# Kernel optimization log

Hardware: AMD Instinct MI355X
Metric: run time of the kernel (lower is better)

## Reference

```python
import jax, jax.numpy as jnp
import numpy as np

EPS = 0.001   # EPSILON2
T1 = 1.0
T2 = 100.0
DISC = 16     # number of discrete features
B, F, K1, K2 = 524288, 16, 16, 8


def _enforce(v):
    # Enforced autograd fn: forward = max(v, EPS), backward = identity (STE)
    return v + jax.lax.stop_gradient(jnp.maximum(v, EPS) - v)


def _soft_bin(cont, interval, i_min):
    """cont: [B,F]; interval: [F,K]; i_min: [F]. Vectorized over features/bins.
    Returns (STE one-hot out [B, F*K], kmeans_loss scalar)."""
    # bin centers = i_min + running cumsum of (enforced) gaps -> [F,K]
    centers = i_min[:, None] + jnp.cumsum(_enforce(interval), axis=1)
    d = (cont[:, :, None] - centers[None, :, :]) ** 2          # [B,F,K]
    s1 = jax.nn.softmax(-T1 * d, axis=-1)                      # kmeans softmax
    kmeans_loss = jnp.sum(jnp.mean(jnp.sum(d * s1, axis=-1), axis=0))
    s2 = jax.nn.softmax(-T2 * d, axis=-1)                      # sharp softmax
    oh = jax.nn.one_hot(jnp.argmax(s2, axis=-1), d.shape[-1], dtype=s2.dtype)
    out = s2 + jax.lax.stop_gradient(oh - s2)                  # STE one-hot
    return out.reshape(cont.shape[0], -1), kmeans_loss


def setup_inputs() -> dict:
    key = jax.random.key(0)
    k1, k2, k3 = jax.random.split(key, 3)
    x = jax.random.uniform(k1, (B, DISC + F), dtype=jnp.float32)
    interval = jax.random.uniform(k2, (F, K1), dtype=jnp.float32,
                                  minval=0.01, maxval=0.12)
    interval2 = jax.random.uniform(k3, (F, K2), dtype=jnp.float32,
                                   minval=0.02, maxval=0.2)
    i_min = jnp.zeros((F,), dtype=jnp.float32)
    return {"x": x, "interval": interval, "interval2": interval2, "i_min": i_min}


def reference(x, interval, interval2, i_min):
    x_disc, cont = x[:, :DISC], x[:, DISC:]
    out1, loss1 = _soft_bin(cont, interval, i_min)
    out2, loss2 = _soft_bin(cont, interval2, i_min)
    total_out = jnp.concatenate([x_disc, out1, out2], axis=1)  # [B, DISC+F*(K1+K2)]
    return total_out, loss1 + loss2
```

## Files before the change

### kernel.cpp

```cpp
#include <hip/hip_runtime.h>


typedef float vfloat4 __attribute__((ext_vector_type(4)));

constexpr int kB      = 524288;
constexpr int kF      = 16;
constexpr int kK1     = 16;
constexpr int kK2     = 8;
constexpr int kRowIn  = 32;
constexpr int kRowOut = 400;
constexpr float kEps  = 0.001f;
constexpr int kTPB    = 256;
constexpr int kGrid   = kB / kTPB;
constexpr int kXStride = 17;

template <int K>
__device__ __forceinline__ int soft_argmax_loss(const float* __restrict__ dd,
                                                double& lacc)
{
#pragma clang fp contract(off)
    float se = 0.f, sde = 0.f;
#pragma unroll
    for (int k = 0; k < K; ++k) {
        float e = __expf(-dd[k]);
        se += e; sde += dd[k] * e;
    }
    lacc += (double)(sde / se);

    float z[K];
#pragma unroll
    for (int k = 0; k < K; ++k) z[k] = -100.0f * dd[k];
    float m = z[0]; int kmax = 0;
#pragma unroll
    for (int k = 1; k < K; ++k) {
        if (z[k] > m) { m = z[k]; kmax = k; }
    }

    bool cand = false;
#pragma unroll
    for (int k = 0; k < K; ++k)
        cand |= (k < kmax) & (z[k] >= m - 2.4e-7f);
    if (cand) {
        float e2[K]; float ss = 0.f;
        for (int k = 0; k < K; ++k) { e2[k] = expf(z[k] - m); ss += e2[k]; }
        int km = 0; float pmax = e2[0] / ss;
        for (int k = 1; k < K; ++k) {
            float p = e2[k] / ss;
            if (p > pmax) { pmax = p; km = k; }
        }
        kmax = km;
    }
    return kmax;
}

__global__ __launch_bounds__(kTPB) void binlayer_main(
    const float* __restrict__ x,
    const float* __restrict__ interval,
    const float* __restrict__ interval2,
    const float* __restrict__ i_min,
    float* __restrict__ out,
    double* __restrict__ partial)
{
#pragma clang fp contract(off)
    __shared__ float sC1[kF][kK1];
    __shared__ float sC2[kF][kK2];
    __shared__ float sCont[kTPB * kXStride];
    __shared__ unsigned char sIdx[kTPB * kF];
    __shared__ double sL[kTPB / 64];

    const int tid = threadIdx.x;

    if (tid < kF) {
        const float base = i_min[tid];
        float run = 0.f;
        for (int k = 0; k < kK1; ++k) {
            run += fmaxf(interval[tid * kK1 + k], kEps);
            sC1[tid][k] = base + run;
        }
        run = 0.f;
        for (int k = 0; k < kK2; ++k) {
            run += fmaxf(interval2[tid * kK2 + k], kEps);
            sC2[tid][k] = base + run;
        }
    }

    const long long rowBase = (long long)blockIdx.x * kTPB;
    const vfloat4* __restrict__ xin4 = (const vfloat4*)(x + rowBase * kRowIn);
    vfloat4* __restrict__ o4 = (vfloat4*)(out + rowBase * kRowOut);

#pragma unroll
    for (int i = 0; i < 4; ++i) {
        int flat = i * kTPB + tid;
        int r = flat >> 2, c = flat & 3;
        vfloat4 v = xin4[r * 8 + 4 + c];
        float* p = &sCont[r * kXStride + c * 4];
        p[0] = v.x; p[1] = v.y; p[2] = v.z; p[3] = v.w;
    }

#pragma unroll
    for (int i = 0; i < 4; ++i) {
        int flat = i * kTPB + tid;
        int r = flat >> 2, c = flat & 3;
        vfloat4 v = xin4[r * 8 + c];
        __builtin_nontemporal_store(v, &o4[r * 100 + c]);
    }

    __syncthreads();

    double lacc = 0.0;
    const float* __restrict__ myc = &sCont[tid * kXStride];

#pragma unroll 1
    for (int f = 0; f < kF; ++f) {
        const float c = myc[f];

        float dd1[kK1];
#pragma unroll
        for (int k = 0; k < kK1; ++k) { float t = c - sC1[f][k]; dd1[k] = t * t; }
        int k1 = soft_argmax_loss<kK1>(dd1, lacc);

        float dd2[kK2];
#pragma unroll
        for (int k = 0; k < kK2; ++k) { float t = c - sC2[f][k]; dd2[k] = t * t; }
        int k2 = soft_argmax_loss<kK2>(dd2, lacc);

        sIdx[tid * kF + f] = (unsigned char)(k1 | (k2 << 4));
    }

#pragma unroll
    for (int off = 32; off > 0; off >>= 1) lacc += __shfl_down(lacc, off);
    if ((tid & 63) == 0) sL[tid >> 6] = lacc;

    __syncthreads();

    if (tid == 0) partial[blockIdx.x] = sL[0] + sL[1] + sL[2] + sL[3];

#pragma unroll 4
    for (int i = 0; i < 96; ++i) {
        unsigned idx = (unsigned)(i * kTPB + tid);
        unsigned r = idx / 96u;
        unsigned c = idx - r * 96u;
        vfloat4 o;
        if (c < 64u) {
            unsigned f = c >> 2, q = (c & 3u) * 4u;
            unsigned k = sIdx[r * kF + f] & 15u;
            o.x = (k == q + 0u) ? 1.f : 0.f;
            o.y = (k == q + 1u) ? 1.f : 0.f;
            o.z = (k == q + 2u) ? 1.f : 0.f;
            o.w = (k == q + 3u) ? 1.f : 0.f;
        } else {
            unsigned u = c - 64u, f = u >> 1, q = (u & 1u) * 4u;
            unsigned k = (unsigned)(sIdx[r * kF + f]) >> 4;
            o.x = (k == q + 0u) ? 1.f : 0.f;
            o.y = (k == q + 1u) ? 1.f : 0.f;
            o.z = (k == q + 2u) ? 1.f : 0.f;
            o.w = (k == q + 3u) ? 1.f : 0.f;
        }
        __builtin_nontemporal_store(o, &o4[r * 100u + 4u + c]);
    }
}

__global__ __launch_bounds__(256) void binlayer_finalize(
    const double* __restrict__ partial,
    float* __restrict__ out)
{
    __shared__ double sL[4];
    const int tid = threadIdx.x;
    double s = 0.0;
#pragma unroll
    for (int i = 0; i < kGrid / 256; ++i)
        s += partial[i * 256 + tid];
#pragma unroll
    for (int off = 32; off > 0; off >>= 1) s += __shfl_down(s, off);
    if ((tid & 63) == 0) sL[tid >> 6] = s;
    __syncthreads();
    if (tid == 0)
        out[(long long)kB * kRowOut] =
            (float)((sL[0] + sL[1] + sL[2] + sL[3]) * (1.0 / (double)kB));
}

extern "C" void kernel_launch(void* const* d_in, const int* in_sizes, int n_in,
                              void* d_out, int out_size, void* d_ws, size_t ws_size,
                              hipStream_t stream)
{
    const float* x    = (const float*)d_in[0];
    const float* itv1 = (const float*)d_in[1];
    const float* itv2 = (const float*)d_in[2];
    const float* imin = (const float*)d_in[3];
    float* out = (float*)d_out;
    double* partial = (double*)d_ws;

    binlayer_main<<<kGrid, kTPB, 0, stream>>>(x, itv1, itv2, imin, out, partial);
    binlayer_finalize<<<1, 256, 0, stream>>>(partial, out);
}
```

Measured before the change: 908.6 us.

## Split compute and one-hot expansion into separate kernels via packed index buffer

Splits the fused kernel into a compute kernel that writes 16 bytes of packed bin indices per row to workspace, and an expand kernel that writes the full contiguous output rows. Each phase can then run at its own occupancy, and the store phase no longer waits on the compute-heavy phase. Output stores become fully contiguous per block, since the x_disc copy is merged into the expansion loop, and they switch from nontemporal to normal stores. The cost is an extra launch, an extra read of x, and 8 MB of round-trip index traffic. A fused fallback is kept for when the workspace is too small.

```diff
diff --git a/kernel.cpp b/kernel.cpp
--- a/kernel.cpp
+++ b/kernel.cpp
@@ -13,6 +13,7 @@
 constexpr int kTPB    = 256;
 constexpr int kGrid   = kB / kTPB;
 constexpr int kXStride = 17;
+constexpr int kWStride = 5;
 
 template <int K>
 __device__ __forceinline__ int soft_argmax_loss(const float* __restrict__ dd,
@@ -35,7 +36,6 @@
     for (int k = 1; k < K; ++k) {
         if (z[k] > m) { m = z[k]; kmax = k; }
     }
-
     bool cand = false;
 #pragma unroll
     for (int k = 0; k < K; ++k)
@@ -53,7 +53,141 @@
     return kmax;
 }
 
-__global__ __launch_bounds__(kTPB) void binlayer_main(
+__device__ __forceinline__ void load_centers(
+    const float* __restrict__ interval, const float* __restrict__ interval2,
+    const float* __restrict__ i_min, int tid,
+    float (*sC1)[kK1], float (*sC2)[kK2])
+{
+#pragma clang fp contract(off)
+    if (tid < kF) {
+        const float base = i_min[tid];
+        float run = 0.f;
+        for (int k = 0; k < kK1; ++k) {
+            run += fmaxf(interval[tid * kK1 + k], kEps);
+            sC1[tid][k] = base + run;
+        }
+        run = 0.f;
+        for (int k = 0; k < kK2; ++k) {
+            run += fmaxf(interval2[tid * kK2 + k], kEps);
+            sC2[tid][k] = base + run;
+        }
+    }
+}
+
+__global__ __launch_bounds__(kTPB) void binlayer_compute(
+    const float* __restrict__ x,
+    const float* __restrict__ interval,
+    const float* __restrict__ interval2,
+    const float* __restrict__ i_min,
+    uint4* __restrict__ idxbuf,
+    double* __restrict__ partial)
+{
+#pragma clang fp contract(off)
+    __shared__ float sC1[kF][kK1];
+    __shared__ float sC2[kF][kK2];
+    __shared__ float sCont[kTPB * kXStride];
+    __shared__ double sL[kTPB / 64];
+
+    const int tid = threadIdx.x;
+    load_centers(interval, interval2, i_min, tid, sC1, sC2);
+
+    const long long rowBase = (long long)blockIdx.x * kTPB;
+    const vfloat4* __restrict__ xin4 = (const vfloat4*)(x + rowBase * kRowIn);
+
+#pragma unroll
+    for (int i = 0; i < 4; ++i) {
+        int flat = i * kTPB + tid;
+        int r = flat >> 2, c = flat & 3;
+        vfloat4 v = xin4[r * 8 + 4 + c];
+        float* p = &sCont[r * kXStride + c * 4];
+        p[0] = v.x; p[1] = v.y; p[2] = v.z; p[3] = v.w;
+    }
+    __syncthreads();
+
+    double lacc = 0.0;
+    const float* __restrict__ myc = &sCont[tid * kXStride];
+    unsigned w[4] = {0u, 0u, 0u, 0u};
+
+#pragma unroll 1
+    for (int f = 0; f < kF; ++f) {
+        const float c = myc[f];
+        float dd1[kK1];
+#pragma unroll
+        for (int k = 0; k < kK1; ++k) { float t = c - sC1[f][k]; dd1[k] = t * t; }
+        int k1 = soft_argmax_loss<kK1>(dd1, lacc);
+        float dd2[kK2];
+#pragma unroll
+        for (int k = 0; k < kK2; ++k) { float t = c - sC2[f][k]; dd2[k] = t * t; }
+        int k2 = soft_argmax_loss<kK2>(dd2, lacc);
+        w[f >> 2] |= (unsigned)(k1 | (k2 << 4)) << (8 * (f & 3));
+    }
+
+    idxbuf[rowBase + tid] = make_uint4(w[0], w[1], w[2], w[3]);
+
+#pragma unroll
+    for (int off = 32; off > 0; off >>= 1) lacc += __shfl_down(lacc, off);
+    if ((tid & 63) == 0) sL[tid >> 6] = lacc;
+    __syncthreads();
+    if (tid == 0) partial[blockIdx.x] = sL[0] + sL[1] + sL[2] + sL[3];
+}
+
+__global__ __launch_bounds__(kTPB) void binlayer_expand(
+    const float* __restrict__ x,
+    const uint4* __restrict__ idxbuf,
+    float* __restrict__ out)
+{
+    __shared__ float sX[kTPB * kXStride];
+    __shared__ unsigned sW[kTPB * kWStride];
+
+    const int tid = threadIdx.x;
+    const long long rowBase = (long long)blockIdx.x * kTPB;
+    const vfloat4* __restrict__ xin4 = (const vfloat4*)(x + rowBase * kRowIn);
+    vfloat4* __restrict__ o4 = (vfloat4*)(out + rowBase * kRowOut);
+
+    {
+        uint4 v = idxbuf[rowBase + tid];
+        unsigned* p = &sW[tid * kWStride];
+        p[0] = v.x; p[1] = v.y; p[2] = v.z; p[3] = v.w;
+    }
+#pragma unroll
+    for (int i = 0; i < 4; ++i) {
+        int flat = i * kTPB + tid;
+        int r = flat >> 2, c = flat & 3;
+        vfloat4 v = xin4[r * 8 + c];
+        float* p = &sX[r * kXStride + c * 4];
+        p[0] = v.x; p[1] = v.y; p[2] = v.z; p[3] = v.w;
+    }
+    __syncthreads();
+
+#pragma unroll 4
+    for (int i = 0; i < 100; ++i) {
+        unsigned idx = (unsigned)(i * kTPB + tid);
+        unsigned r = idx / 100u;
+        unsigned c = idx - r * 100u;
+        vfloat4 o;
+        if (c < 4u) {
+            const float* p = &sX[r * kXStride + c * 4u];
+            o.x = p[0]; o.y = p[1]; o.z = p[2]; o.w = p[3];
+        } else if (c < 68u) {
+            unsigned u = c - 4u, f = u >> 2, q = (u & 3u) * 4u;
+            unsigned k = (sW[r * kWStride + (f >> 2)] >> (8u * (f & 3u))) & 15u;
+            o.x = (k == q + 0u) ? 1.f : 0.f;
+            o.y = (k == q + 1u) ? 1.f : 0.f;
+            o.z = (k == q + 2u) ? 1.f : 0.f;
+            o.w = (k == q + 3u) ? 1.f : 0.f;
+        } else {
+            unsigned u = c - 68u, f = u >> 1, q = (u & 1u) * 4u;
+            unsigned k = (sW[r * kWStride + (f >> 2)] >> (8u * (f & 3u) + 4u)) & 15u;
+            o.x = (k == q + 0u) ? 1.f : 0.f;
+            o.y = (k == q + 1u) ? 1.f : 0.f;
+            o.z = (k == q + 2u) ? 1.f : 0.f;
+            o.w = (k == q + 3u) ? 1.f : 0.f;
+        }
+        o4[idx] = o;
+    }
+}
+
+__global__ __launch_bounds__(kTPB) void binlayer_fused(
     const float* __restrict__ x,
     const float* __restrict__ interval,
     const float* __restrict__ interval2,
@@ -64,99 +198,72 @@
 #pragma clang fp contract(off)
     __shared__ float sC1[kF][kK1];
     __shared__ float sC2[kF][kK2];
-    __shared__ float sCont[kTPB * kXStride];
+    __shared__ float sX[kTPB * 33];
     __shared__ unsigned char sIdx[kTPB * kF];
     __shared__ double sL[kTPB / 64];
 
     const int tid = threadIdx.x;
-
-    if (tid < kF) {
-        const float base = i_min[tid];
-        float run = 0.f;
-        for (int k = 0; k < kK1; ++k) {
-            run += fmaxf(interval[tid * kK1 + k], kEps);
-            sC1[tid][k] = base + run;
-        }
-        run = 0.f;
-        for (int k = 0; k < kK2; ++k) {
-            run += fmaxf(interval2[tid * kK2 + k], kEps);
-            sC2[tid][k] = base + run;
-        }
-    }
+    load_centers(interval, interval2, i_min, tid, sC1, sC2);
 
     const long long rowBase = (long long)blockIdx.x * kTPB;
     const vfloat4* __restrict__ xin4 = (const vfloat4*)(x + rowBase * kRowIn);
-    vfloat4* __restrict__ o4 = (vfloat4*)(out + rowBase * kRowOut);
-
-#pragma unroll
-    for (int i = 0; i < 4; ++i) {
+#pragma unroll
+    for (int i = 0; i < 8; ++i) {
         int flat = i * kTPB + tid;
-        int r = flat >> 2, c = flat & 3;
-        vfloat4 v = xin4[r * 8 + 4 + c];
-        float* p = &sCont[r * kXStride + c * 4];
+        vfloat4 v = xin4[flat];
+        int r = flat >> 3, c4 = flat & 7;
+        float* p = &sX[r * 33 + c4 * 4];
         p[0] = v.x; p[1] = v.y; p[2] = v.z; p[3] = v.w;
     }
-
-#pragma unroll
-    for (int i = 0; i < 4; ++i) {
-        int flat = i * kTPB + tid;
-        int r = flat >> 2, c = flat & 3;
-        vfloat4 v = xin4[r * 8 + c];
-        __builtin_nontemporal_store(v, &o4[r * 100 + c]);
-    }
-
     __syncthreads();
 
     double lacc = 0.0;
-    const float* __restrict__ myc = &sCont[tid * kXStride];
-
+    const float* __restrict__ myc = &sX[tid * 33 + 16];
 #pragma unroll 1
     for (int f = 0; f < kF; ++f) {
         const float c = myc[f];
-
         float dd1[kK1];
 #pragma unroll
         for (int k = 0; k < kK1; ++k) { float t = c - sC1[f][k]; dd1[k] = t * t; }
         int k1 = soft_argmax_loss<kK1>(dd1, lacc);
-
         float dd2[kK2];
 #pragma unroll
         for (int k = 0; k < kK2; ++k) { float t = c - sC2[f][k]; dd2[k] = t * t; }
         int k2 = soft_argmax_loss<kK2>(dd2, lacc);
-
         sIdx[tid * kF + f] = (unsigned char)(k1 | (k2 << 4));
     }
-
 #pragma unroll
     for (int off = 32; off > 0; off >>= 1) lacc += __shfl_down(lacc, off);
     if ((tid & 63) == 0) sL[tid >> 6] = lacc;
-
-    __syncthreads();
-
+    __syncthreads();
     if (tid == 0) partial[blockIdx.x] = sL[0] + sL[1] + sL[2] + sL[3];
 
-#pragma unroll 4
-    for (int i = 0; i < 96; ++i) {
+    vfloat4* __restrict__ o4 = (vfloat4*)(out + rowBase * kRowOut);
+#pragma unroll 1
+    for (int i = 0; i < 100; ++i) {
         unsigned idx = (unsigned)(i * kTPB + tid);
-        unsigned r = idx / 96u;
-        unsigned c = idx - r * 96u;
+        unsigned r = idx / 100u;
+        unsigned c = idx - r * 100u;
         vfloat4 o;
-        if (c < 64u) {
-            unsigned f = c >> 2, q = (c & 3u) * 4u;
+        if (c < 4u) {
+            const float* p = &sX[r * 33 + c * 4u];
+            o.x = p[0]; o.y = p[1]; o.z = p[2]; o.w = p[3];
+        } else if (c < 68u) {
+            unsigned u = c - 4u, f = u >> 2, q = (u & 3u) * 4u;
             unsigned k = sIdx[r * kF + f] & 15u;
             o.x = (k == q + 0u) ? 1.f : 0.f;
             o.y = (k == q + 1u) ? 1.f : 0.f;
             o.z = (k == q + 2u) ? 1.f : 0.f;
             o.w = (k == q + 3u) ? 1.f : 0.f;
         } else {
-            unsigned u = c - 64u, f = u >> 1, q = (u & 1u) * 4u;
+            unsigned u = c - 68u, f = u >> 1, q = (u & 1u) * 4u;
             unsigned k = (unsigned)(sIdx[r * kF + f]) >> 4;
             o.x = (k == q + 0u) ? 1.f : 0.f;
             o.y = (k == q + 1u) ? 1.f : 0.f;
             o.z = (k == q + 2u) ? 1.f : 0.f;
             o.w = (k == q + 3u) ? 1.f : 0.f;
         }
-        __builtin_nontemporal_store(o, &o4[r * 100u + 4u + c]);
+        o4[idx] = o;
     }
 }
 
@@ -188,8 +295,18 @@
     const float* itv2 = (const float*)d_in[2];
     const float* imin = (const float*)d_in[3];
     float* out = (float*)d_out;
+
     double* partial = (double*)d_ws;
-
-    binlayer_main<<<kGrid, kTPB, 0, stream>>>(x, itv1, itv2, imin, out, partial);
+    uint4* idxbuf = (uint4*)((char*)d_ws + kGrid * sizeof(double));
+    const size_t need = kGrid * sizeof(double) + (size_t)kB * sizeof(uint4);
+
+    if (ws_size >= need) {
+        binlayer_compute<<<kGrid, kTPB, 0, stream>>>(x, itv1, itv2, imin,
+                                                     idxbuf, partial);
+        binlayer_expand<<<kGrid, kTPB, 0, stream>>>(x, idxbuf, out);
+    } else {
+        binlayer_fused<<<kGrid, kTPB, 0, stream>>>(x, itv1, itv2, imin,
+                                                   out, partial);
+    }
     binlayer_finalize<<<1, 256, 0, stream>>>(partial, out);
 }
```

After: 954.6 us. +5.1%, slower.

## Make each wave independent: per-wave smem staging, packed indices, per-wave partials

Applied to the files above, without the earlier changes.

Restructures the block so each 64-lane wave stages its own rows in shared memory and emits its own one-hot output. This removes the block-wide barrier between compute and store and the cross-wave reduction of the loss. Indices are packed into 32-bit words per lane instead of byte stores. The finalize kernel now sums four partials per block, and the nontemporal stores are replaced with regular stores, which may change cache behaviour for this write-heavy kernel.

```diff
diff --git a/kernel.cpp b/kernel.cpp
--- a/kernel.cpp
+++ b/kernel.cpp
@@ -12,6 +12,7 @@
 constexpr float kEps  = 0.001f;
 constexpr int kTPB    = 256;
 constexpr int kGrid   = kB / kTPB;
+constexpr int kNPart  = kGrid * 4;
 constexpr int kXStride = 17;
 
 template <int K>
@@ -35,7 +36,6 @@
     for (int k = 1; k < K; ++k) {
         if (z[k] > m) { m = z[k]; kmax = k; }
     }
-
     bool cand = false;
 #pragma unroll
     for (int k = 0; k < K; ++k)
@@ -64,11 +64,30 @@
 #pragma clang fp contract(off)
     __shared__ float sC1[kF][kK1];
     __shared__ float sC2[kF][kK2];
-    __shared__ float sCont[kTPB * kXStride];
-    __shared__ unsigned char sIdx[kTPB * kF];
-    __shared__ double sL[kTPB / 64];
-
-    const int tid = threadIdx.x;
+    __shared__ float sCont[4][64 * kXStride];
+    __shared__ unsigned sW[4][64 * 4];
+
+    const int tid  = threadIdx.x;
+    const int wave = tid >> 6;
+    const int lane = tid & 63;
+
+    const long long waveRow = (long long)blockIdx.x * kTPB + wave * 64;
+    const vfloat4* __restrict__ xin4 = (const vfloat4*)(x + waveRow * kRowIn);
+    vfloat4* __restrict__ o4 = (vfloat4*)(out + waveRow * kRowOut);
+
+    vfloat4 cv[4];
+#pragma unroll
+    for (int i = 0; i < 4; ++i) {
+        int flat = i * 64 + lane;
+        int r = flat >> 2, c = flat & 3;
+        cv[i] = xin4[r * 8 + 4 + c];
+    }
+#pragma unroll
+    for (int i = 0; i < 4; ++i) {
+        int flat = i * 64 + lane;
+        int r = flat >> 2, c = flat & 3;
+        o4[r * 100 + c] = xin4[r * 8 + c];
+    }
 
     if (tid < kF) {
         const float base = i_min[tid];
@@ -83,80 +102,66 @@
             sC2[tid][k] = base + run;
         }
     }
-
-    const long long rowBase = (long long)blockIdx.x * kTPB;
-    const vfloat4* __restrict__ xin4 = (const vfloat4*)(x + rowBase * kRowIn);
-    vfloat4* __restrict__ o4 = (vfloat4*)(out + rowBase * kRowOut);
-
+    __syncthreads();
+
+    float* __restrict__ wc = sCont[wave];
 #pragma unroll
     for (int i = 0; i < 4; ++i) {
-        int flat = i * kTPB + tid;
+        int flat = i * 64 + lane;
         int r = flat >> 2, c = flat & 3;
-        vfloat4 v = xin4[r * 8 + 4 + c];
-        float* p = &sCont[r * kXStride + c * 4];
-        p[0] = v.x; p[1] = v.y; p[2] = v.z; p[3] = v.w;
-    }
-
-#pragma unroll
-    for (int i = 0; i < 4; ++i) {
-        int flat = i * kTPB + tid;
-        int r = flat >> 2, c = flat & 3;
-        vfloat4 v = xin4[r * 8 + c];
-        __builtin_nontemporal_store(v, &o4[r * 100 + c]);
-    }
-
-    __syncthreads();
+        float* p = &wc[r * kXStride + c * 4];
+        p[0] = cv[i].x; p[1] = cv[i].y; p[2] = cv[i].z; p[3] = cv[i].w;
+    }
 
     double lacc = 0.0;
-    const float* __restrict__ myc = &sCont[tid * kXStride];
+    const float* __restrict__ myc = &wc[lane * kXStride];
+    unsigned w[4] = {0u, 0u, 0u, 0u};
 
 #pragma unroll 1
     for (int f = 0; f < kF; ++f) {
         const float c = myc[f];
-
         float dd1[kK1];
 #pragma unroll
         for (int k = 0; k < kK1; ++k) { float t = c - sC1[f][k]; dd1[k] = t * t; }
         int k1 = soft_argmax_loss<kK1>(dd1, lacc);
-
         float dd2[kK2];
 #pragma unroll
         for (int k = 0; k < kK2; ++k) { float t = c - sC2[f][k]; dd2[k] = t * t; }
         int k2 = soft_argmax_loss<kK2>(dd2, lacc);
-
-        sIdx[tid * kF + f] = (unsigned char)(k1 | (k2 << 4));
+        w[f >> 2] |= (unsigned)(k1 | (k2 << 4)) << (8 * (f & 3));
+    }
+    {
+        unsigned* p = &sW[wave][lane * 4];
+        p[0] = w[0]; p[1] = w[1]; p[2] = w[2]; p[3] = w[3];
     }
 
 #pragma unroll
     for (int off = 32; off > 0; off >>= 1) lacc += __shfl_down(lacc, off);
-    if ((tid & 63) == 0) sL[tid >> 6] = lacc;
-
-    __syncthreads();
-
-    if (tid == 0) partial[blockIdx.x] = sL[0] + sL[1] + sL[2] + sL[3];
-
+    if (lane == 0) partial[blockIdx.x * 4 + wave] = lacc;
+
+    const unsigned* __restrict__ ww = sW[wave];
 #pragma unroll 4
     for (int i = 0; i < 96; ++i) {
-        unsigned idx = (unsigned)(i * kTPB + tid);
+        unsigned idx = (unsigned)(i * 64 + lane);
         unsigned r = idx / 96u;
         unsigned c = idx - r * 96u;
         vfloat4 o;
         if (c < 64u) {
             unsigned f = c >> 2, q = (c & 3u) * 4u;
-            unsigned k = sIdx[r * kF + f] & 15u;
+            unsigned k = (ww[r * 4u + (f >> 2)] >> (8u * (f & 3u))) & 15u;
             o.x = (k == q + 0u) ? 1.f : 0.f;
             o.y = (k == q + 1u) ? 1.f : 0.f;
             o.z = (k == q + 2u) ? 1.f : 0.f;
             o.w = (k == q + 3u) ? 1.f : 0.f;
         } else {
             unsigned u = c - 64u, f = u >> 1, q = (u & 1u) * 4u;
-            unsigned k = (unsigned)(sIdx[r * kF + f]) >> 4;
+            unsigned k = (ww[r * 4u + (f >> 2)] >> (8u * (f & 3u) + 4u)) & 15u;
             o.x = (k == q + 0u) ? 1.f : 0.f;
             o.y = (k == q + 1u) ? 1.f : 0.f;
             o.z = (k == q + 2u) ? 1.f : 0.f;
             o.w = (k == q + 3u) ? 1.f : 0.f;
         }
-        __builtin_nontemporal_store(o, &o4[r * 100u + 4u + c]);
+        o4[r * 100u + 4u + c] = o;
     }
 }
 
@@ -168,7 +173,7 @@
     const int tid = threadIdx.x;
     double s = 0.0;
 #pragma unroll
-    for (int i = 0; i < kGrid / 256; ++i)
+    for (int i = 0; i < kNPart / 256; ++i)
         s += partial[i * 256 + tid];
 #pragma unroll
     for (int off = 32; off > 0; off >>= 1) s += __shfl_down(s, off);
```

After: 953.1 us. 4.9% more time.
